# Performance work log

Measured on AMD Instinct MI355X. Metric: run time of the kernel, lower is better.

## Reference

```python
import jax, jax.numpy as jnp
import numpy as np

N = 50000   # nodes
E = 800000  # edges
F = 128     # input features
W = 128     # hidden width
K = 5       # Chebyshev order


def setup_inputs() -> dict:
    key = jax.random.key(0)
    ks = jax.random.split(key, 12)
    x = jax.random.normal(ks[0], (N, F), jnp.float32)
    edge_index = jax.random.randint(ks[1], (2, E), 0, N, jnp.int32)
    def p(i, shape):
        return jax.random.normal(ks[i], shape, jnp.float32) * 0.05
    return {
        'x': x,
        'edge_index': edge_index,
        'W0': p(2, (K, F, W)), 'b0': p(3, (W,)),
        'W1': p(4, (K, W, W)), 'b1': p(5, (W,)),
        'W2': p(6, (K, W, W)), 'b2': p(7, (W,)),
        'Wl': p(8, (W, 1)),   'bl': p(9, (1,)),
    }


def _norm(edge_index):
    # PyG ChebConv norm with lambda_max=2.0, sym normalization:
    # Lhat = 2/lambda_max * (I - D^-1/2 A D^-1/2) - I  ->  diag 0, offdiag -d_r*d_c
    src, dst = edge_index[0], edge_index[1]
    ew = (src != dst).astype(jnp.float32)  # remove self loops
    deg = jax.ops.segment_sum(ew, src, num_segments=N)
    dinv = jnp.where(deg > 0, jax.lax.rsqrt(jnp.maximum(deg, 1.0)), 0.0)
    w = -ew * dinv[src] * dinv[dst]
    return src, dst, w


def _cheb_conv(h, Wk, b, src, dst, w):
    # Tx_0 = h; Tx_1 = Lhat h; Tx_k = 2 Lhat Tx_{k-1} - Tx_{k-2}
    def matvec(v):
        # gather from src, weight, scatter-add to dst: [E, C] message tensor
        return jax.ops.segment_sum(w[:, None] * v[src], dst, num_segments=N)
    Tx0 = h
    out = Tx0 @ Wk[0]
    Tx1 = matvec(Tx0)
    out = out + Tx1 @ Wk[1]
    for k in range(2, Wk.shape[0]):
        Tx2 = 2.0 * matvec(Tx1) - Tx0
        out = out + Tx2 @ Wk[k]
        Tx0, Tx1 = Tx1, Tx2
    return out + b


def reference(x, edge_index, W0, b0, W1, b1, W2, b2, Wl, bl):
    src, dst, w = _norm(edge_index)
    h = jax.nn.relu(_cheb_conv(x, W0, b0, src, dst, w))  # dropout = identity (eval)
    h = jax.nn.relu(_cheb_conv(h, W1, b1, src, dst, w))
    h = _cheb_conv(h, W2, b2, src, dst, w)
    return h @ Wl + bl  # [N, 1]
```

## Files before the change

kernel.cpp:

```cpp
#include <hip/hip_runtime.h>
#include <hip/hip_bf16.h>
#include <stdint.h>

#define N_NODES 50000
#define N_EDGES 800000
#define FEAT 128
#define CAP 64
#define NCVT 1600000
#define NTRW 163840
#define NPRE (NCVT + NTRW + N_EDGES)

typedef __attribute__((ext_vector_type(4))) float floatx4;
typedef __attribute__((ext_vector_type(8))) _Float16 half8;
typedef __attribute__((ext_vector_type(4))) _Float16 half4;

__device__ __forceinline__ float bf2f(unsigned short u) {
  union { unsigned u; float f; } v; v.u = ((unsigned)u) << 16; return v.f;
}
__device__ __forceinline__ unsigned short f2bf(float f) {
  union { float f; unsigned u; } v; v.f = f;
  unsigned r = v.u + 0x7fffu + ((v.u >> 16) & 1u);
  return (unsigned short)(r >> 16);
}
__device__ __forceinline__ unsigned pack_edge(float w, int s) {
  _Float16 h = (_Float16)w;
  unsigned short hb = __builtin_bit_cast(unsigned short, h);
  return ((unsigned)s << 16) | (unsigned)hb;
}
__device__ __forceinline__ float edge_w(unsigned e) {
  unsigned short hb = (unsigned short)(e & 0xFFFFu);
  return (float)__builtin_bit_cast(_Float16, hb);
}
__device__ __forceinline__ int edge_src(unsigned e) { return (int)(e >> 16); }

__global__ void k_pre1(const unsigned short* __restrict__ x,
                       const void* b0, const void* b1, const void* b2,
                       const void* wl, const void* bl,
                       float* __restrict__ pf, int* __restrict__ flag) {
  __shared__ int cnt_s;
  __shared__ int fl_s;
  int tid = threadIdx.x;
  if (tid == 0) cnt_s = 0;
  __syncthreads();
  int big = 0;
  for (int i = tid; i < 4096; i += 256) {
    unsigned short u = x[2 * i];
    int e = (u >> 7) & 0xFF;
    if (e >= 0xE0) big++;
  }
  atomicAdd(&cnt_s, big);
  __syncthreads();
  if (tid == 0) { fl_s = (cnt_s > 16) ? 1 : 0; flag[0] = fl_s; }
  __syncthreads();
  int fl = fl_s;
  for (int i = tid; i < 513; i += 256) {
    const void* src; int off;
    if (i < 128)      { src = b0; off = i; }
    else if (i < 256) { src = b1; off = i - 128; }
    else if (i < 384) { src = b2; off = i - 256; }
    else if (i < 512) { src = wl; off = i - 384; }
    else              { src = bl; off = 0; }
    pf[i] = fl ? ((const float*)src)[off] : bf2f(((const unsigned short*)src)[off]);
  }
}

__global__ void k_prev(const void* __restrict__ w2, float* __restrict__ pf,
                       const int* __restrict__ flag) {
  int d = blockIdx.x * 256 + threadIdx.x;
  if (d > 640) return;
  int fl = flag[0];
  if (d < 640) {
    int k = d >> 7, f = d & 127;
    float s = 0.f;
    const int base = (k << 14) + (f << 7);
    if (fl) {
      const float* w = (const float*)w2 + base;
#pragma unroll 8
      for (int i = 0; i < 128; ++i) s += w[i] * pf[384 + i];
    } else {
      const unsigned short* w = (const unsigned short*)w2 + base;
#pragma unroll 8
      for (int i = 0; i < 128; ++i) s += bf2f(w[i]) * pf[384 + i];
    }
    pf[520 + d] = s;
  } else {
    float s = 0.f;
    for (int i = 0; i < 128; ++i) s += pf[256 + i] * pf[384 + i];
    pf[1160] = s + pf[512];
  }
}

__global__ void k_pre2(const void* __restrict__ xp,
                       const void* __restrict__ w0, const void* __restrict__ w1,
                       const int* __restrict__ esrc, const int* __restrict__ edst,
                       _Float16* __restrict__ t0, _Float16* __restrict__ wt,
                       int* __restrict__ deg,
                       const int* __restrict__ flag) {
  int i = blockIdx.x * blockDim.x + threadIdx.x;
  int fl = flag[0];
  if (i < NCVT) {
    float4 o;
    if (fl) {
      o = ((const float4*)xp)[i];
    } else {
      ushort4 v = ((const ushort4*)xp)[i];
      o.x = bf2f(v.x); o.y = bf2f(v.y); o.z = bf2f(v.z); o.w = bf2f(v.w);
    }
    half4 h;
    h[0] = (_Float16)o.x; h[1] = (_Float16)o.y; h[2] = (_Float16)o.z; h[3] = (_Float16)o.w;
    ((half4*)t0)[i] = h;
  } else if (i < NCVT + NTRW) {
    int tid = i - NCVT;
    int li = tid >> 14;
    int r = tid & 16383;
    int n = r >> 7, kk = r & 127;
    int l = li / 5, k = li - l * 5;
    const void* w = (l == 0) ? w0 : w1;
    int idx = k * 16384 + kk * 128 + n;
    float v = fl ? ((const float*)w)[idx] : bf2f(((const unsigned short*)w)[idx]);
    wt[tid] = (_Float16)v;
  } else {
    int e = i - (NCVT + NTRW);
    if (e >= N_EDGES) return;
    int s = esrc[e], d = edst[e];
    if (s != d) atomicAdd(&deg[s], 1);
  }
}

__global__ __launch_bounds__(256) void k_quant(const _Float16* __restrict__ X,
                                               unsigned char* __restrict__ Q,
                                               float* __restrict__ S) {
  int wave = threadIdx.x >> 6, lane = threadIdx.x & 63;
  int q = lane >> 4, l16 = lane & 15;
  int node = blockIdx.x * 16 + wave * 4 + q;
  if (node >= N_NODES) return;
  half8 h = ((const half8*)(X + (size_t)node * FEAT))[l16];
  float v[8], mx = 0.f;
#pragma unroll
  for (int f = 0; f < 8; ++f) { v[f] = (float)h[f]; mx = fmaxf(mx, fabsf(v[f])); }
#pragma unroll
  for (int o = 1; o < 16; o <<= 1) mx = fmaxf(mx, __shfl_xor(mx, o));
  float inv = mx > 0.f ? 127.f / mx : 0.f;
  int qb[8];
#pragma unroll
  for (int f = 0; f < 8; ++f) qb[f] = (int)rintf(v[f] * inv) + 128;
  uint2 p;
  p.x = (unsigned)qb[0] | ((unsigned)qb[1] << 8) | ((unsigned)qb[2] << 16) | ((unsigned)qb[3] << 24);
  p.y = (unsigned)qb[4] | ((unsigned)qb[5] << 8) | ((unsigned)qb[6] << 16) | ((unsigned)qb[7] << 24);
  ((uint2*)(Q + (size_t)node * FEAT))[l16] = p;
  if (l16 == 0) S[node] = mx > 0.f ? mx / 127.f : 0.f;
}

__global__ void k_fill(const int* __restrict__ src, const int* __restrict__ dst,
                       const int* __restrict__ deg,
                       int* __restrict__ cnt, unsigned* __restrict__ edata) {
  int e = blockIdx.x * blockDim.x + threadIdx.x;
  if (e >= N_EDGES) return;
  int s = src[e], d = dst[e];
  if (s == d) return;
  int ds = deg[s], dd = deg[d];
  float w = (ds > 0 && dd > 0) ? -rsqrtf((float)ds) * rsqrtf((float)dd) : 0.f;
  int pos = atomicAdd(&cnt[d], 1);
  if (pos < CAP) edata[(d << 6) + pos] = pack_edge(w, s);
}

__global__ __launch_bounds__(256) void k_spmv(const unsigned* __restrict__ edata,
                                              const int* __restrict__ cnt,
                                              const unsigned char* __restrict__ Q,
                                              const float* __restrict__ S,
                                              const _Float16* __restrict__ Z,
                                              _Float16* __restrict__ Y,
                                              unsigned char* __restrict__ Qo,
                                              float* __restrict__ So,
                                              float alpha, int hasZ, int wshadow) {
  int wave = threadIdx.x >> 6, lane = threadIdx.x & 63;
  int q = lane >> 4, l16 = lane & 15;
  int node = blockIdx.x * 16 + wave * 4 + q;
  if (node >= N_NODES) return;
  int n_e = cnt[node]; if (n_e > CAP) n_e = CAP;
  int base = node << 6;

  float acc[8];
#pragma unroll
  for (int f = 0; f < 8; ++f) acc[f] = 0.f;
  float wsum = 0.f;

  unsigned e0 = (0 < n_e) ? edata[base + 0] : 0u;
  unsigned e1 = (1 < n_e) ? edata[base + 1] : 0u;
  unsigned e2 = (2 < n_e) ? edata[base + 2] : 0u;
  unsigned e3 = (3 < n_e) ? edata[base + 3] : 0u;
  unsigned e4 = (4 < n_e) ? edata[base + 4] : 0u;
  unsigned e5 = (5 < n_e) ? edata[base + 5] : 0u;
  unsigned e6 = (6 < n_e) ? edata[base + 6] : 0u;
  unsigned e7 = (7 < n_e) ? edata[base + 7] : 0u;
  uint2 r0 = ((const uint2*)(Q + (size_t)edge_src(e0) * FEAT))[l16];
  uint2 r1 = ((const uint2*)(Q + (size_t)edge_src(e1) * FEAT))[l16];
  uint2 r2 = ((const uint2*)(Q + (size_t)edge_src(e2) * FEAT))[l16];
  uint2 r3 = ((const uint2*)(Q + (size_t)edge_src(e3) * FEAT))[l16];
  float s0 = S[edge_src(e0)], s1 = S[edge_src(e1)], s2 = S[edge_src(e2)], s3 = S[edge_src(e3)];

  for (int j = 0; j < n_e; j += 4) {
    float ws0 = edge_w(e0) * s0, ws1 = edge_w(e1) * s1;
    float ws2 = edge_w(e2) * s2, ws3 = edge_w(e3) * s3;
    uint2 c0 = r0, c1 = r1, c2 = r2, c3 = r3;
    e0 = e4; e1 = e5; e2 = e6; e3 = e7;
    e4 = (j + 8 < n_e) ? edata[base + j + 8] : 0u;
    e5 = (j + 9 < n_e) ? edata[base + j + 9] : 0u;
    e6 = (j + 10 < n_e) ? edata[base + j + 10] : 0u;
    e7 = (j + 11 < n_e) ? edata[base + j + 11] : 0u;
    r0 = ((const uint2*)(Q + (size_t)edge_src(e0) * FEAT))[l16];
    r1 = ((const uint2*)(Q + (size_t)edge_src(e1) * FEAT))[l16];
    r2 = ((const uint2*)(Q + (size_t)edge_src(e2) * FEAT))[l16];
    r3 = ((const uint2*)(Q + (size_t)edge_src(e3) * FEAT))[l16];
    s0 = S[edge_src(e0)]; s1 = S[edge_src(e1)]; s2 = S[edge_src(e2)]; s3 = S[edge_src(e3)];
#define DEC8(c, w)                                                        \
    acc[0] = fmaf(w, (float)(c.x & 0xFFu), acc[0]);                       \
    acc[1] = fmaf(w, (float)((c.x >> 8) & 0xFFu), acc[1]);                \
    acc[2] = fmaf(w, (float)((c.x >> 16) & 0xFFu), acc[2]);               \
    acc[3] = fmaf(w, (float)(c.x >> 24), acc[3]);                         \
    acc[4] = fmaf(w, (float)(c.y & 0xFFu), acc[4]);                       \
    acc[5] = fmaf(w, (float)((c.y >> 8) & 0xFFu), acc[5]);                \
    acc[6] = fmaf(w, (float)((c.y >> 16) & 0xFFu), acc[6]);               \
    acc[7] = fmaf(w, (float)(c.y >> 24), acc[7]);
    DEC8(c0, ws0) DEC8(c1, ws1) DEC8(c2, ws2) DEC8(c3, ws3)
#undef DEC8
    wsum += (ws0 + ws1) + (ws2 + ws3);
  }
  float rx[8];
  float b128 = 128.f * wsum;
  if (hasZ) {
    half8 z = ((const half8*)(Z + (size_t)node * FEAT))[l16];
#pragma unroll
    for (int f = 0; f < 8; ++f) rx[f] = fmaf(alpha, acc[f] - b128, -(float)z[f]);
  } else {
#pragma unroll
    for (int f = 0; f < 8; ++f) rx[f] = alpha * (acc[f] - b128);
  }
  half8 res;
#pragma unroll
  for (int f = 0; f < 8; ++f) res[f] = (_Float16)rx[f];
  ((half8*)(Y + (size_t)node * FEAT))[l16] = res;
  if (wshadow) {
    float mx = 0.f;
#pragma unroll
    for (int f = 0; f < 8; ++f) mx = fmaxf(mx, fabsf(rx[f]));
#pragma unroll
    for (int o = 1; o < 16; o <<= 1) mx = fmaxf(mx, __shfl_xor(mx, o));
    float inv = mx > 0.f ? 127.f / mx : 0.f;
    int qb[8];
#pragma unroll
    for (int f = 0; f < 8; ++f) qb[f] = (int)rintf(rx[f] * inv) + 128;
    uint2 p;
    p.x = (unsigned)qb[0] | ((unsigned)qb[1] << 8) | ((unsigned)qb[2] << 16) | ((unsigned)qb[3] << 24);
    p.y = (unsigned)qb[4] | ((unsigned)qb[5] << 8) | ((unsigned)qb[6] << 16) | ((unsigned)qb[7] << 24);
    ((uint2*)(Qo + (size_t)node * FEAT))[l16] = p;
    if (l16 == 0) So[node] = mx > 0.f ? mx / 127.f : 0.f;
  }
}

__global__ __launch_bounds__(256) void k_smv(const unsigned* __restrict__ edata,
                                             const int* __restrict__ cnt,
                                             const float* __restrict__ h,
                                             const float* __restrict__ b,
                                             const float* __restrict__ bprev,
                                             float cL, float* __restrict__ y,
                                             int is_out, void* __restrict__ outp,
                                             const int* __restrict__ flag,
                                             const float* __restrict__ cptr) {
  int wave = threadIdx.x >> 6, lane = threadIdx.x & 63;
  int q = lane >> 4, l16 = lane & 15;
  int node = blockIdx.x * 16 + wave * 4 + q;
  if (node >= N_NODES) return;
  int n_e = cnt[node]; if (n_e > CAP) n_e = CAP;
  int base = node << 6;
  float s = 0.f;
  for (int j = l16; j < n_e; j += 16) {
    unsigned e = edata[base + j];
    s = fmaf(edge_w(e), b[edge_src(e)], s);
  }
#pragma unroll
  for (int o = 1; o < 16; o <<= 1) s += __shfl_xor(s, o);
  if (l16 == 0) {
    float r = fmaf(cL, s, h[node]) - (bprev ? bprev[node] : 0.f);
    if (!is_out) {
      y[node] = r;
    } else {
      r += cptr[0];
      if (flag[0]) ((float*)outp)[node] = r;
      else ((unsigned short*)outp)[node] = f2bf(r);
    }
  }
}

__global__ __launch_bounds__(256) void k_gemm(const _Float16* __restrict__ t0, const _Float16* __restrict__ t1,
                                              const _Float16* __restrict__ t2, const _Float16* __restrict__ t3,
                                              const _Float16* __restrict__ t4,
                                              const _Float16* __restrict__ wt,
                                              const float* __restrict__ bias,
                                              _Float16* __restrict__ dst, int mode,
                                              const float* __restrict__ v0,
                                              float* __restrict__ hout,
                                              unsigned char* __restrict__ q8,
                                              float* __restrict__ sc) {
  __shared__ _Float16 lb[128 * 136];
  const _Float16* tp[5] = {t0, t1, t2, t3, t4};
  int tid = threadIdx.x, wave = tid >> 6, lane = tid & 63;
  int quad = lane >> 4, l16 = lane & 15;
  int m0 = blockIdx.x * 128;
  floatx4 acc[2][8];
#pragma unroll
  for (int s = 0; s < 2; ++s)
#pragma unroll
    for (int j = 0; j < 8; ++j) acc[s][j] = (floatx4){0.f, 0.f, 0.f, 0.f};
  int arow[2];
  bool aval[2];
#pragma unroll
  for (int s = 0; s < 2; ++s) {
    arow[s] = m0 + wave * 32 + s * 16 + l16;
    aval[s] = arow[s] < N_NODES;
  }

#pragma unroll
  for (int k = 0; k < 5; ++k) {
    __syncthreads();
    {
      int n = tid >> 1, half = tid & 1;
      const uint4* sp = (const uint4*)(wt + k * 16384 + n * 128 + half * 64);
      uint4* dq = (uint4*)(lb + n * 136 + half * 64);
#pragma unroll
      for (int i = 0; i < 8; ++i) dq[i] = sp[i];
    }
    __syncthreads();
    const _Float16* A = tp[k];
#pragma unroll
    for (int ki = 0; ki < 4; ++ki) {
      half8 af[2];
#pragma unroll
      for (int s = 0; s < 2; ++s) {
        if (aval[s]) {
          af[s] = *((const half8*)(A + (size_t)arow[s] * FEAT + ki * 32 + quad * 8));
        } else {
#pragma unroll
          for (int i = 0; i < 8; ++i) af[s][i] = (_Float16)0.f;
        }
      }
#pragma unroll
      for (int j = 0; j < 8; ++j) {
        half8 bf = *((const half8*)(lb + (j * 16 + l16) * 136 + ki * 32 + quad * 8));
        acc[0][j] = __builtin_amdgcn_mfma_f32_16x16x32_f16(af[0], bf, acc[0][j], 0, 0, 0);
        acc[1][j] = __builtin_amdgcn_mfma_f32_16x16x32_f16(af[1], bf, acc[1][j], 0, 0, 0);
      }
    }
  }
#pragma unroll
  for (int s = 0; s < 2; ++s) {
    int rbase = m0 + wave * 32 + s * 16 + quad * 4;
    if (mode == 0) {
      float mx[4] = {0.f, 0.f, 0.f, 0.f};
#pragma unroll
      for (int j = 0; j < 8; ++j) {
        int col = j * 16 + l16;
        float b = bias[col];
#pragma unroll
        for (int r = 0; r < 4; ++r) {
          int m = rbase + r;
          float v = fmaxf(acc[s][j][r] + b, 0.f);
          if (m < N_NODES) dst[(size_t)m * FEAT + col] = (_Float16)v;
          mx[r] = fmaxf(mx[r], v);
        }
      }
#pragma unroll
      for (int o = 1; o < 16; o <<= 1) {
#pragma unroll
        for (int r = 0; r < 4; ++r) mx[r] = fmaxf(mx[r], __shfl_xor(mx[r], o));
      }
      float inv[4];
#pragma unroll
      for (int r = 0; r < 4; ++r) inv[r] = mx[r] > 0.f ? 127.f / mx[r] : 0.f;
      if (l16 == 0) {
#pragma unroll
        for (int r = 0; r < 4; ++r) {
          int m = rbase + r;
          if (m < N_NODES) sc[m] = mx[r] > 0.f ? mx[r] / 127.f : 0.f;
        }
      }
#pragma unroll
      for (int j = 0; j < 8; ++j) {
        int col = j * 16 + l16;
        float b = bias[col];
#pragma unroll
        for (int r = 0; r < 4; ++r) {
          int m = rbase + r;
          if (m < N_NODES) {
            float v = fmaxf(acc[s][j][r] + b, 0.f);
            int qv = (int)rintf(v * inv[r]) + 128;
            q8[(size_t)m * FEAT + col] = (unsigned char)qv;
          }
        }
      }
    } else {
      float p[5][4];
#pragma unroll
      for (int k = 0; k < 5; ++k)
#pragma unroll
        for (int r = 0; r < 4; ++r) p[k][r] = 0.f;
#pragma unroll
      for (int j = 0; j < 8; ++j) {
        int col = j * 16 + l16;
        float b = bias[col];
        float vv[5];
#pragma unroll
        for (int k = 0; k < 5; ++k) vv[k] = v0[k * 128 + col];
#pragma unroll
        for (int r = 0; r < 4; ++r) {
          float val = fmaxf(acc[s][j][r] + b, 0.f);
#pragma unroll
          for (int k = 0; k < 5; ++k) p[k][r] = fmaf(val, vv[k], p[k][r]);
        }
      }
#pragma unroll
      for (int o = 1; o < 16; o <<= 1) {
#pragma unroll
        for (int k = 0; k < 5; ++k)
#pragma unroll
          for (int r = 0; r < 4; ++r) p[k][r] += __shfl_xor(p[k][r], o);
      }
      if (l16 == 0) {
#pragma unroll
        for (int r = 0; r < 4; ++r) {
          int m = rbase + r;
          if (m < N_NODES) {
#pragma unroll
            for (int k = 0; k < 5; ++k) hout[k * N_NODES + m] = p[k][r];
          }
        }
      }
    }
  }
}

extern "C" void kernel_launch(void* const* d_in, const int* in_sizes, int n_in,
                              void* d_out, int out_size, void* d_ws, size_t ws_size,
                              hipStream_t stream) {
  const void* x  = d_in[0];
  const int* ei  = (const int*)d_in[1];
  const void* w0 = d_in[2];
  const void* b0 = d_in[3];
  const void* w1 = d_in[4];
  const void* b1 = d_in[5];
  const void* w2 = d_in[6];
  const void* b2 = d_in[7];
  const void* wl = d_in[8];
  const void* bl = d_in[9];
  const int* src = ei;
  const int* dst = ei + N_EDGES;

  char* ws = (char*)d_ws;
  size_t off = 0;
  auto alloc = [&](size_t bytes) -> char* {
    char* p = ws + off;
    off += (bytes + 255) & ~(size_t)255;
    return p;
  };
  _Float16* T[5];
  for (int i = 0; i < 5; ++i) T[i] = (_Float16*)alloc(sizeof(_Float16) * N_NODES * FEAT);
  unsigned char* Q[5];
  for (int i = 0; i < 5; ++i) Q[i] = (unsigned char*)alloc((size_t)N_NODES * FEAT);
  float* S[5];
  for (int i = 0; i < 5; ++i) S[i] = (float*)alloc(sizeof(float) * N_NODES);
  unsigned* edata = (unsigned*)alloc(sizeof(unsigned) * N_NODES * CAP);
  int* cnt = (int*)alloc(sizeof(int) * N_NODES * 2);
  int* deg = cnt + N_NODES;
  _Float16* wt = (_Float16*)alloc(sizeof(_Float16) * NTRW);
  float* pf = (float*)alloc(sizeof(float) * 1536);
  float* hbuf = (float*)alloc(sizeof(float) * 5 * N_NODES);
  float* bbuf = (float*)alloc(sizeof(float) * 3 * N_NODES);
  int* flag = (int*)alloc(sizeof(int));

  hipMemsetAsync(cnt, 0, sizeof(int) * N_NODES * 2, stream);
  k_pre1<<<1, 256, 0, stream>>>((const unsigned short*)x, b0, b1, b2, wl, bl, pf, flag);
  k_prev<<<3, 256, 0, stream>>>(w2, pf, flag);
  k_pre2<<<(NPRE + 255) / 256, 256, 0, stream>>>(x, w0, w1, src, dst, T[0], wt, deg, flag);

  int nblk_spmv = (N_NODES + 15) / 16;
  int nblk_gemm = (N_NODES + 127) / 128;
  k_quant<<<nblk_spmv, 256, 0, stream>>>(T[0], Q[0], S[0]);
  k_fill<<<(N_EDGES + 255) / 256, 256, 0, stream>>>(src, dst, deg, cnt, edata);

  const float* v = pf + 520;
  const float* cc = pf + 1160;

  for (int l = 0; l < 2; ++l) {
    k_spmv<<<nblk_spmv, 256, 0, stream>>>(edata, cnt, Q[0], S[0], nullptr, T[1], Q[1], S[1], 1.f, 0, 1);
    k_spmv<<<nblk_spmv, 256, 0, stream>>>(edata, cnt, Q[1], S[1], T[0], T[2], Q[2], S[2], 2.f, 1, 1);
    k_spmv<<<nblk_spmv, 256, 0, stream>>>(edata, cnt, Q[2], S[2], T[1], T[3], Q[3], S[3], 2.f, 1, 1);
    k_spmv<<<nblk_spmv, 256, 0, stream>>>(edata, cnt, Q[3], S[3], T[2], T[4], nullptr, nullptr, 2.f, 1, 0);
    k_gemm<<<nblk_gemm, 256, 0, stream>>>(T[0], T[1], T[2], T[3], T[4],
                                          wt + l * 5 * 16384, pf + l * 128, T[0],
                                          l, v, hbuf, Q[0], S[0]);
  }
  float* h0 = hbuf;
  float* h1 = hbuf + N_NODES;
  float* h2 = hbuf + 2 * N_NODES;
  float* h3 = hbuf + 3 * N_NODES;
  float* h4 = hbuf + 4 * N_NODES;
  float* b3 = bbuf;
  float* b2c = bbuf + N_NODES;
  float* b1c = bbuf + 2 * N_NODES;
  k_smv<<<nblk_spmv, 256, 0, stream>>>(edata, cnt, h3, h4, nullptr, 2.f, b3, 0, nullptr, flag, nullptr);
  k_smv<<<nblk_spmv, 256, 0, stream>>>(edata, cnt, h2, b3, h4, 2.f, b2c, 0, nullptr, flag, nullptr);
  k_smv<<<nblk_spmv, 256, 0, stream>>>(edata, cnt, h1, b2c, b3, 2.f, b1c, 0, nullptr, flag, nullptr);
  k_smv<<<nblk_spmv, 256, 0, stream>>>(edata, cnt, h0, b1c, b2c, 1.f, nullptr, 1, d_out, flag, cc);
}
```

Measured before the change: 454.7 us.

## Partition degree and fill atomics by XCD node range; fuse quantization into convert

```diff
diff --git a/kernel.cpp b/kernel.cpp
--- a/kernel.cpp
+++ b/kernel.cpp
@@ -8,7 +8,9 @@
 #define CAP 64
 #define NCVT 1600000
 #define NTRW 163840
-#define NPRE (NCVT + NTRW + N_EDGES)
+#define NPRE (NCVT + NTRW)
+#define NXCD 8
+#define RNG 6250
 
 typedef __attribute__((ext_vector_type(4))) float floatx4;
 typedef __attribute__((ext_vector_type(8))) _Float16 half8;
@@ -92,9 +94,9 @@
 
 __global__ void k_pre2(const void* __restrict__ xp,
                        const void* __restrict__ w0, const void* __restrict__ w1,
-                       const int* __restrict__ esrc, const int* __restrict__ edst,
-                       _Float16* __restrict__ t0, _Float16* __restrict__ wt,
-                       int* __restrict__ deg,
+                       _Float16* __restrict__ t0,
+                       unsigned char* __restrict__ q0, float* __restrict__ s0,
+                       _Float16* __restrict__ wt,
                        const int* __restrict__ flag) {
   int i = blockIdx.x * blockDim.x + threadIdx.x;
   int fl = flag[0];
@@ -109,8 +111,19 @@
     half4 h;
     h[0] = (_Float16)o.x; h[1] = (_Float16)o.y; h[2] = (_Float16)o.z; h[3] = (_Float16)o.w;
     ((half4*)t0)[i] = h;
-  } else if (i < NCVT + NTRW) {
+    float mx = fmaxf(fmaxf(fabsf(o.x), fabsf(o.y)), fmaxf(fabsf(o.z), fabsf(o.w)));
+#pragma unroll
+    for (int d = 1; d < 32; d <<= 1) mx = fmaxf(mx, __shfl_xor(mx, d));
+    float inv = mx > 0.f ? 127.f / mx : 0.f;
+    int qa = (int)rintf(o.x * inv) + 128;
+    int qb = (int)rintf(o.y * inv) + 128;
+    int qc = (int)rintf(o.z * inv) + 128;
+    int qd = (int)rintf(o.w * inv) + 128;
+    ((unsigned*)q0)[i] = (unsigned)qa | ((unsigned)qb << 8) | ((unsigned)qc << 16) | ((unsigned)qd << 24);
+    if ((i & 31) == 0) s0[i >> 5] = mx > 0.f ? mx / 127.f : 0.f;
+  } else {
     int tid = i - NCVT;
+    if (tid >= NTRW) return;
     int li = tid >> 14;
     int r = tid & 16383;
     int n = r >> 7, kk = r & 127;
@@ -119,49 +132,41 @@
     int idx = k * 16384 + kk * 128 + n;
     float v = fl ? ((const float*)w)[idx] : bf2f(((const unsigned short*)w)[idx]);
     wt[tid] = (_Float16)v;
-  } else {
-    int e = i - (NCVT + NTRW);
-    if (e >= N_EDGES) return;
-    int s = esrc[e], d = edst[e];
-    if (s != d) atomicAdd(&deg[s], 1);
-  }
-}
-
-__global__ __launch_bounds__(256) void k_quant(const _Float16* __restrict__ X,
-                                               unsigned char* __restrict__ Q,
-                                               float* __restrict__ S) {
-  int wave = threadIdx.x >> 6, lane = threadIdx.x & 63;
-  int q = lane >> 4, l16 = lane & 15;
-  int node = blockIdx.x * 16 + wave * 4 + q;
-  if (node >= N_NODES) return;
-  half8 h = ((const half8*)(X + (size_t)node * FEAT))[l16];
-  float v[8], mx = 0.f;
-#pragma unroll
-  for (int f = 0; f < 8; ++f) { v[f] = (float)h[f]; mx = fmaxf(mx, fabsf(v[f])); }
-#pragma unroll
-  for (int o = 1; o < 16; o <<= 1) mx = fmaxf(mx, __shfl_xor(mx, o));
-  float inv = mx > 0.f ? 127.f / mx : 0.f;
-  int qb[8];
-#pragma unroll
-  for (int f = 0; f < 8; ++f) qb[f] = (int)rintf(v[f] * inv) + 128;
-  uint2 p;
-  p.x = (unsigned)qb[0] | ((unsigned)qb[1] << 8) | ((unsigned)qb[2] << 16) | ((unsigned)qb[3] << 24);
-  p.y = (unsigned)qb[4] | ((unsigned)qb[5] << 8) | ((unsigned)qb[6] << 16) | ((unsigned)qb[7] << 24);
-  ((uint2*)(Q + (size_t)node * FEAT))[l16] = p;
-  if (l16 == 0) S[node] = mx > 0.f ? mx / 127.f : 0.f;
-}
-
-__global__ void k_fill(const int* __restrict__ src, const int* __restrict__ dst,
-                       const int* __restrict__ deg,
-                       int* __restrict__ cnt, unsigned* __restrict__ edata) {
-  int e = blockIdx.x * blockDim.x + threadIdx.x;
-  if (e >= N_EDGES) return;
-  int s = src[e], d = dst[e];
-  if (s == d) return;
-  int ds = deg[s], dd = deg[d];
-  float w = (ds > 0 && dd > 0) ? -rsqrtf((float)ds) * rsqrtf((float)dd) : 0.f;
-  int pos = atomicAdd(&cnt[d], 1);
-  if (pos < CAP) edata[(d << 6) + pos] = pack_edge(w, s);
+  }
+}
+
+__global__ __launch_bounds__(256) void k_deg8(const int* __restrict__ src,
+                                              const int* __restrict__ dst,
+                                              int* __restrict__ deg) {
+  int g = blockIdx.x & 7;
+  int lo = g * RNG, hi = lo + RNG; if (hi > N_NODES) hi = N_NODES;
+  int nb = gridDim.x >> 3;
+  int bi = blockIdx.x >> 3;
+  for (int e = bi * 256 + threadIdx.x; e < N_EDGES; e += nb * 256) {
+    int s = src[e];
+    if (s >= lo && s < hi && s != dst[e]) atomicAdd(&deg[s], 1);
+  }
+}
+
+__global__ __launch_bounds__(256) void k_fill8(const int* __restrict__ src,
+                                               const int* __restrict__ dst,
+                                               const int* __restrict__ deg,
+                                               int* __restrict__ cnt,
+                                               unsigned* __restrict__ edata) {
+  int g = blockIdx.x & 7;
+  int lo = g * RNG, hi = lo + RNG; if (hi > N_NODES) hi = N_NODES;
+  int nb = gridDim.x >> 3;
+  int bi = blockIdx.x >> 3;
+  for (int e = bi * 256 + threadIdx.x; e < N_EDGES; e += nb * 256) {
+    int d = dst[e];
+    if (d < lo || d >= hi) continue;
+    int s = src[e];
+    if (s == d) continue;
+    int ds = deg[s], dd = deg[d];
+    float w = (ds > 0 && dd > 0) ? -rsqrtf((float)ds) * rsqrtf((float)dd) : 0.f;
+    int pos = atomicAdd(&cnt[d], 1);
+    if (pos < CAP) edata[(d << 6) + pos] = pack_edge(w, s);
+  }
 }
 
 __global__ __launch_bounds__(256) void k_spmv(const unsigned* __restrict__ edata,
@@ -480,13 +485,12 @@
   hipMemsetAsync(cnt, 0, sizeof(int) * N_NODES * 2, stream);
   k_pre1<<<1, 256, 0, stream>>>((const unsigned short*)x, b0, b1, b2, wl, bl, pf, flag);
   k_prev<<<3, 256, 0, stream>>>(w2, pf, flag);
-  k_pre2<<<(NPRE + 255) / 256, 256, 0, stream>>>(x, w0, w1, src, dst, T[0], wt, deg, flag);
+  k_pre2<<<(NPRE + 255) / 256, 256, 0, stream>>>(x, w0, w1, T[0], Q[0], S[0], wt, flag);
+  k_deg8<<<512, 256, 0, stream>>>(src, dst, deg);
+  k_fill8<<<512, 256, 0, stream>>>(src, dst, deg, cnt, edata);
 
   int nblk_spmv = (N_NODES + 15) / 16;
   int nblk_gemm = (N_NODES + 127) / 128;
-  k_quant<<<nblk_spmv, 256, 0, stream>>>(T[0], Q[0], S[0]);
-  k_fill<<<(N_EDGES + 255) / 256, 256, 0, stream>>>(src, dst, deg, cnt, edata);
-
   const float* v = pf + 520;
   const float* cc = pf + 1160;
 
```

Measured after the change: 484.4 us. 1.07x slower.
